# Performance work log

Hardware: AMD Instinct MI355X
Metric: run time of the kernel (lower is better)

## Reference

```python
import jax, jax.numpy as jnp
import numpy as np
import math

E = 65536        # neighbor pairs (edges)
NAT = 2048       # atoms
NRAD = 24        # radial basis size
ZETA = [1, 2, 3, 4]
NCOMP = len(ZETA) + 1  # radial components: one 2-body + one per zeta
RCUT = 6.0
NELEM = 94       # one-hot element encoding size
EMB = 16         # species embedding dim


def _tables():
    """Static lxlylz enumeration per zeta: triples with lx+ly+lz = n, n in 0..z,
    multinomial/binomial normalization and (-1)^n lambda sign."""
    f = np.vectorize(math.factorial)
    tabs = []
    for z in ZETA:
        L = []
        for n in range(z + 1):
            for lx in range(n + 1):
                for ly in range(n - lx + 1):
                    L.append((lx, ly, n - lx - ly))
        L = np.array(L, np.int64)              # [K,3]
        nsum = L.sum(1)                        # [K]
        fact_lxlylz = f(L[:, 0]) * f(L[:, 1]) * f(L[:, 2])
        # (nfact/fact_lxlylz) * z!/((z-n)! n!) = z! / ((z-n)! * lx!ly!lz!)
        fact_norm = math.factorial(z) / (f(z - nsum) * fact_lxlylz)
        lam = (-1.0) ** nsum
        tabs.append((jnp.asarray(L, jnp.float32),
                     jnp.asarray(fact_norm, jnp.float32),
                     jnp.asarray(lam, jnp.float32)))
    return tabs

TABS = _tables()


def _forward(rij, Wr1, br1, Wr2, br2, Ws1, bs1, Ws2, bs2,
             Wa1, ba1, Wa2, ba2, Wa3, ba3, first_atom_idx, species_idx):
    nat = species_idx.shape[0]
    r = jnp.linalg.norm(rij, axis=1)                       # [E]
    u = rij / r[:, None]                                   # [E,3] unit vectors
    fc = 0.5 * (jnp.cos(jnp.pi * jnp.minimum(r, RCUT) / RCUT) + 1.0)
    centers = jnp.linspace(0.0, RCUT, NRAD, dtype=jnp.float32)
    width = RCUT / NRAD
    basis = jnp.exp(-((r[:, None] - centers) ** 2) / (2.0 * width * width)) * fc[:, None]  # [E,NRAD]
    # learned radial functions -> [E, NRAD, NCOMP]
    h = jax.nn.silu(basis @ Wr1 + br1)
    radial = jax.nn.silu(h @ Wr2 + br2).reshape(-1, NRAD, NCOMP)
    seg = first_atom_idx
    # two-body descriptor
    feats = [jax.ops.segment_sum(radial[:, :, 0], seg, num_segments=nat)]  # [nat,NRAD]
    for iz, z in enumerate(ZETA):
        L, fnorm, lam = TABS[iz]
        # g_ij over lxlylz combos: prod of powers of unit-vector components
        g_ij = jnp.prod((u[:, None, :] + 1e-12) ** L[None, :, :], axis=-1) * fnorm  # [E,K]
        g = jnp.einsum('er,ek->erk', radial[:, :, iz + 1], g_ij)                    # [E,NRAD,K]
        gi = jax.ops.segment_sum(g, seg, num_segments=nat)                          # [nat,NRAD,K]
        g2 = gi * gi
        norm = 2.0 ** (1.0 - z)
        feats.append(jnp.sum(g2, axis=-1) * norm)          # lambda = +1
        feats.append(jnp.sum(g2 * lam, axis=-1) * norm)    # lambda = -1
    feat = jnp.concatenate(feats, axis=1)                  # [nat, NRAD*(1+2*nzeta)]
    # species embedding and correlation
    onehot = jax.nn.one_hot(species_idx, NELEM, dtype=feat.dtype)
    emb = jax.nn.silu(onehot @ Ws1 + bs1) @ Ws2 + bs2      # [nat,EMB]
    x = (feat[:, :, None] * emb[:, None, :]).reshape(nat, -1)  # [nat, F*EMB]
    h = jax.nn.silu(x @ Wa1 + ba1)
    h = jax.nn.silu(h @ Wa2 + ba2)
    e = h @ Wa3 + ba3                                      # [nat,1] atomic energies
    return jnp.sum(e)                                      # total energy


def setup_inputs() -> dict:
    key = jax.random.key(0)
    ks = jax.random.split(key, 12)
    def w(k, shp):
        return jax.random.normal(k, shp, jnp.float32) / np.float32(np.sqrt(shp[0]))
    F = NRAD * (1 + 2 * len(ZETA)) * EMB  # 3456
    return {
        "rij": jax.random.normal(ks[0], (E, 3), jnp.float32) * 2.0,
        "Wr1": w(ks[1], (NRAD, 64)), "br1": jnp.zeros((64,), jnp.float32),
        "Wr2": w(ks[2], (64, NCOMP * NRAD)), "br2": jnp.zeros((NCOMP * NRAD,), jnp.float32),
        "Ws1": w(ks[3], (NELEM, 32)), "bs1": jnp.zeros((32,), jnp.float32),
        "Ws2": w(ks[4], (32, EMB)), "bs2": jnp.zeros((EMB,), jnp.float32),
        "Wa1": w(ks[5], (F, 256)), "ba1": jnp.zeros((256,), jnp.float32),
        "Wa2": w(ks[6], (256, 128)), "ba2": jnp.zeros((128,), jnp.float32),
        "Wa3": w(ks[7], (128, 1)), "ba3": jnp.zeros((1,), jnp.float32),
        "first_atom_idx": jnp.sort(jax.random.randint(ks[8], (E,), 0, NAT)),
        "species_idx": jax.random.randint(ks[9], (NAT,), 0, NELEM),
    }


def reference(rij, Wr1, br1, Wr2, br2, Ws1, bs1, Ws2, bs2,
              Wa1, ba1, Wa2, ba2, Wa3, ba3, first_atom_idx, species_idx):
    return _forward(rij, Wr1, br1, Wr2, br2, Ws1, bs1, Ws2, bs2,
                    Wa1, ba1, Wa2, ba2, Wa3, ba3, first_atom_idx, species_idx)
```

## Files before the change

### kernel.cpp

```cpp
#include <hip/hip_runtime.h>
#include <math.h>

#define KTOT 69
#define NRADC 24
#define NFEAT 216
#define NELEMC 94
#define EMBC 16
#define H1C 256
#define H2C 128
#define CE 16
#define EPR 20
#define KGN 18
#define GSTR 84
#define GISTR 76
#define TA 8
#define NPT 344

__device__ __constant__ int c_lx[KTOT] = {
  0,0,0,1,
  0,0,0,1,0,0,0,1,1,2,
  0,0,0,1,0,0,0,1,1,2,0,0,0,0,1,1,1,2,2,3,
  0,0,0,1,0,0,0,1,1,2,0,0,0,0,1,1,1,2,2,3,0,0,0,0,0,1,1,1,1,2,2,2,3,3,4};
__device__ __constant__ int c_ly[KTOT] = {
  0,0,1,0,
  0,0,1,0,0,1,2,0,1,0,
  0,0,1,0,0,1,2,0,1,0,0,1,2,3,0,1,2,0,1,0,
  0,0,1,0,0,1,2,0,1,0,0,1,2,3,0,1,2,0,1,0,0,1,2,3,4,0,1,2,3,0,1,2,0,1,0};
__device__ __constant__ int c_lz[KTOT] = {
  0,1,0,0,
  0,1,0,0,2,1,0,1,0,0,
  0,1,0,0,2,1,0,1,0,0,3,2,1,0,2,1,0,1,0,0,
  0,1,0,0,2,1,0,1,0,0,3,2,1,0,2,1,0,1,0,0,4,3,2,1,0,3,2,1,0,2,1,0,1,0,0};
__device__ __constant__ float c_fn[KTOT] = {
  1,1,1,1,
  1,2,2,2,1,2,1,2,2,1,
  1,3,3,3,3,6,3,6,6,3,1,3,3,1,3,6,3,3,3,1,
  1,4,4,4,6,12,6,12,12,6,4,12,12,4,12,24,12,12,12,4,
  1,4,6,4,1,4,12,12,4,6,12,6,4,4,1};
__device__ __constant__ float c_lam[KTOT] = {
  1,-1,-1,-1,
  1,-1,-1,-1,1,1,1,1,1,1,
  1,-1,-1,-1,1,1,1,1,1,1,-1,-1,-1,-1,-1,-1,-1,-1,-1,-1,
  1,-1,-1,-1,1,1,1,1,1,1,-1,-1,-1,-1,-1,-1,-1,-1,-1,-1,
  1,1,1,1,1,1,1,1,1,1,1,1,1,1,1};
__device__ __constant__ int c_k0[4] = {0,4,14,34};
__device__ __constant__ int c_kn[4] = {4,10,20,35};
__device__ __constant__ float c_zn[4] = {1.0f, 0.5f, 0.25f, 0.125f};
__device__ __constant__ int c_zidg[KGN] = {0, 1,1,1, 2,2,2,2,2, 3,3,3,3,3,3,3,3,3};

__device__ __forceinline__ float silu(float x) { return x / (1.0f + expf(-x)); }
__device__ __forceinline__ float4 silu4(float4 v) {
  v.x = silu(v.x); v.y = silu(v.y); v.z = silu(v.z); v.w = silu(v.w); return v;
}
__device__ __forceinline__ void fma4(float4& a, float s, const float4 w) {
  a.x += s * w.x; a.y += s * w.y; a.z += s * w.z; a.w += s * w.w;
}
__device__ __forceinline__ void fma44(float4& a, const float4 x, const float4 y) {
  a.x += x.x * y.x; a.y += x.y * y.y; a.z += x.z * y.z; a.w += x.w * y.w;
}
__device__ __forceinline__ float hsum4(const float4 v) { return (v.x + v.y) + (v.z + v.w); }
__device__ __forceinline__ float powsel(int l, float p, float p2, float p3, float p4) {
  float v = 1.0f;
  v = l >= 1 ? p : v;
  v = l >= 2 ? p2 : v;
  v = l >= 3 ? p3 : v;
  v = l >= 4 ? p4 : v;
  return v;
}

__global__ __launch_bounds__(256) void k_prep(
    const int* __restrict__ fai, const int* __restrict__ spc,
    const float* __restrict__ Ws1, const float* __restrict__ bs1,
    const float* __restrict__ Ws2, const float* __restrict__ bs2,
    const float* __restrict__ Wa1,
    int* __restrict__ bounds, int* __restrict__ porder,
    float* __restrict__ B, int E, int nat, int nbB) {
  const int blk = blockIdx.x;
  const int tid = threadIdx.x;
  __shared__ float s_hh[24 * 32];
  __shared__ float s_emb[24 * EMBC];
  __shared__ int s_cnt[NELEMC];
  __shared__ int s_off[NELEMC];

  if (blk < nbB) {
    int e = blk * 256 + tid;
    if (e < E) {
      int f = fai[e];
      int fp = (e == 0) ? -1 : fai[e - 1];
      for (int a = fp + 1; a <= f; ++a) bounds[a] = e;
      if (e == E - 1)
        for (int a = f + 1; a <= nat; ++a) bounds[a] = E;
    }
  } else if (blk == nbB) {
    for (int i = tid; i < NELEMC; i += 256) s_cnt[i] = 0;
    __syncthreads();
    for (int a = tid; a < nat; a += 256) atomicAdd(&s_cnt[spc[a]], 1);
    __syncthreads();
    if (tid == 0) {
      int run = 0;
      for (int s = 0; s < NELEMC; ++s) {
        s_off[s] = run;
        run += ((s_cnt[s] + TA - 1) / TA) * TA;
      }
    }
    for (int i = tid; i < NPT * TA; i += 256) porder[i] = -1;
    __syncthreads();
    for (int a = tid; a < nat; a += 256) {
      int pos = atomicAdd(&s_off[spc[a]], 1);
      porder[pos] = a;
    }
  } else {
    const int bi = blk - nbB - 1;
    const int i = bi >> 2;
    const int sc0 = (bi & 3) * 24;
    const int scn = min(NELEMC, sc0 + 24) - sc0;
    const int o = tid;
    for (int idx = tid; idx < scn * 32; idx += 256) {
      int s = idx >> 5, c = idx & 31;
      s_hh[idx] = silu(Ws1[(sc0 + s) * 32 + c] + bs1[c]);
    }
    __syncthreads();
    for (int idx = tid; idx < scn * EMBC; idx += 256) {
      int s = idx >> 4, j = idx & 15;
      float acc = bs2[j];
      #pragma unroll
      for (int c = 0; c < 32; ++c) acc += s_hh[s * 32 + c] * Ws2[c * EMBC + j];
      s_emb[idx] = acc;
    }
    __syncthreads();
    float w[EMBC];
    #pragma unroll
    for (int j = 0; j < EMBC; ++j) w[j] = Wa1[(size_t)(i * EMBC + j) * H1C + o];
    for (int s = 0; s < scn; ++s) {
      float acc = 0.0f;
      #pragma unroll
      for (int j = 0; j < EMBC; ++j) acc += s_emb[s * EMBC + j] * w[j];
      B[((size_t)(sc0 + s) * NFEAT + i) * H1C + o] = acc;
    }
  }
}

template <int NQ>
__device__ __forceinline__ void edge_l2(
    const float* __restrict__ s_h, const float* __restrict__ Wr2,
    const float* __restrict__ br2, float4* __restrict__ radial4,
    int e, int og, int eg, int E) {
  float4 acc[NQ];
  const float4* b2 = (const float4*)(br2 + og * 32);
  #pragma unroll
  for (int q = 0; q < NQ; ++q) acc[q] = b2[q];
  #pragma unroll 8
  for (int j = 0; j < 64; ++j) {
    float hv = s_h[e * 65 + j];
    const float4* w = (const float4*)(Wr2 + j * 120 + og * 32);
    #pragma unroll
    for (int q = 0; q < NQ; ++q) fma4(acc[q], hv, w[q]);
  }
  if (eg < E) {
    #pragma unroll
    for (int q = 0; q < NQ; ++q)
      radial4[(size_t)eg * 30 + og * 8 + q] = silu4(acc[q]);
  }
}

__global__ __launch_bounds__(256) void k_edge(
    const float* __restrict__ rij,
    const float* __restrict__ Wr1, const float* __restrict__ br1,
    const float* __restrict__ Wr2, const float* __restrict__ br2,
    float4* __restrict__ radial4, int E) {
  __shared__ float s_bas[64 * 25];
  __shared__ float s_h[64 * 65];
  const int tid = threadIdx.x;
  const int e = tid & 63;
  const int og = __builtin_amdgcn_readfirstlane(tid >> 6);
  const int eg = blockIdx.x * 64 + e;

  {
    float x = 0.0f, y = 0.0f, z = 0.0f;
    const bool ev = eg < E;
    if (ev) { x = rij[3 * eg]; y = rij[3 * eg + 1]; z = rij[3 * eg + 2]; }
    float r = sqrtf(x * x + y * y + z * z);
    float fcv = ev ? 0.5f * (cosf(3.14159265358979323846f * fminf(r, 6.0f) *
                                  (1.0f / 6.0f)) + 1.0f)
                   : 0.0f;
    #pragma unroll
    for (int t = 0; t < 6; ++t) {
      int m = og * 6 + t;
      float d = r - (6.0f / 23.0f) * (float)m;
      s_bas[e * 25 + m] = expf(-8.0f * d * d) * fcv;
    }
  }
  __syncthreads();

  {
    const float4* b1 = (const float4*)(br1 + og * 16);
    float4 acc[4] = {b1[0], b1[1], b1[2], b1[3]};
    #pragma unroll 8
    for (int m = 0; m < NRADC; ++m) {
      float b = s_bas[e * 25 + m];
      const float4* w = (const float4*)(Wr1 + m * 64 + og * 16);
      #pragma unroll
      for (int q = 0; q < 4; ++q) fma4(acc[q], b, w[q]);
    }
    #pragma unroll
    for (int q = 0; q < 4; ++q) {
      float4 v = silu4(acc[q]);
      float* dst = &s_h[e * 65 + og * 16 + 4 * q];
      dst[0] = v.x; dst[1] = v.y; dst[2] = v.z; dst[3] = v.w;
    }
  }
  __syncthreads();

  if (og < 3) edge_l2<8>(s_h, Wr2, br2, radial4, e, og, eg, E);
  else        edge_l2<6>(s_h, Wr2, br2, radial4, e, og, eg, E);
}

__global__ __launch_bounds__(256) void k_atom(
    const float* __restrict__ rij,
    const float4* __restrict__ radial4,
    const int* __restrict__ bounds,
    float* __restrict__ feat, int E) {
  const int a = blockIdx.x;
  const int tid = threadIdx.x;
  __shared__ __align__(16) float s_radT[120 * EPR];
  __shared__ __align__(16) float s_gijT[KGN * GSTR];
  __shared__ __align__(16) float s_gi[NRADC * GISTR];
  __shared__ float s_feat[NFEAT];

  const int start = bounds[a];
  const int end = bounds[a + 1];

  const int e = tid & 15;
  const int sub = tid >> 4;

  const bool is_tile = tid < 216;
  const int eh = (tid < 216) ? (tid / 108) : 0;
  const int tile = (tid < 216) ? (tid % 108) : 0;
  const int rg = tile % 6;
  const int kg = tile / 6;
  const int comp0 = rg * 20 + 1 + c_zidg[kg];
  const bool is_2b = (tid >= 216 && tid < 240);
  const int rad2b = tid - 216;

  const int kstart = sub < 5 ? sub * 5 : 25 + (sub - 5) * 4;
  const int kcnt = sub < 5 ? 5 : 4;
  int t_pk[5], t_addr[5]; float t_fn[5];
  #pragma unroll
  for (int t = 0; t < 5; ++t) {
    int k = (t < kcnt) ? kstart + t : 0;
    t_pk[t] = c_lx[k] | (c_ly[k] << 8) | (c_lz[k] << 16);
    t_fn[t] = c_fn[k];
    int prow = k + (k < 14 ? 0 : 2);
    t_addr[t] = (prow >> 2) * GSTR + (prow & 3) * EPR + e;
  }

  const int pe0 = tid / 30, pc0 = tid - pe0 * 30;
  const int pe1 = (tid + 256) / 30, pc1 = (tid + 256) - pe1 * 30;

  if (tid < 60) {
    int rr = tid / EPR, ec = tid % EPR;
    int fkg = rr < 2 ? 3 : 17;
    int fj = rr < 2 ? 2 + rr : 3;
    s_gijT[fkg * GSTR + fj * EPR + ec] = 0.0f;
  }

  float4 acc[4][4];
  #pragma unroll
  for (int i = 0; i < 4; ++i)
    #pragma unroll
    for (int j = 0; j < 4; ++j) acc[i][j] = make_float4(0, 0, 0, 0);
  float4 acc2b = make_float4(0, 0, 0, 0);

  float4 pfA, pfB;
  float rx, ry, rz;
  auto prefetch = [&](int c0) {
    int lim = (end - c0) * 30;
    pfA = make_float4(0, 0, 0, 0);
    pfB = make_float4(0, 0, 0, 0);
    if (tid < lim) pfA = radial4[(size_t)c0 * 30 + tid];
    if (tid < 224 && tid + 256 < lim) pfB = radial4[(size_t)c0 * 30 + 256 + tid];
    int eg = c0 + e;
    rx = 0.0f; ry = 0.0f; rz = 0.0f;
    if (eg < end) { rx = rij[3 * eg]; ry = rij[3 * eg + 1]; rz = rij[3 * eg + 2]; }
  };
  prefetch(start);

  for (int c0 = start; c0 < end; c0 += CE) {
    __syncthreads();
    {
      int c = pc0 * 4;
      s_radT[(c + 0) * EPR + pe0] = pfA.x;
      s_radT[(c + 1) * EPR + pe0] = pfA.y;
      s_radT[(c + 2) * EPR + pe0] = pfA.z;
      s_radT[(c + 3) * EPR + pe0] = pfA.w;
      if (tid < 224) {
        int c2 = pc1 * 4;
        s_radT[(c2 + 0) * EPR + pe1] = pfB.x;
        s_radT[(c2 + 1) * EPR + pe1] = pfB.y;
        s_radT[(c2 + 2) * EPR + pe1] = pfB.z;
        s_radT[(c2 + 3) * EPR + pe1] = pfB.w;
      }
    }
    {
      const bool ev = (c0 + e) < end;
      float r = sqrtf(rx * rx + ry * ry + rz * rz);
      float inv = 1.0f / r;
      float px = rx * inv + 1e-12f, py = ry * inv + 1e-12f, pz = rz * inv + 1e-12f;
      float p2x = px * px, p3x = p2x * px, p4x = p2x * p2x;
      float p2y = py * py, p3y = p2y * py, p4y = p2y * p2y;
      float p2z = pz * pz, p3z = p2z * pz, p4z = p2z * p2z;
      #pragma unroll
      for (int t = 0; t < 5; ++t) {
        if (t < kcnt) {
          int pk = t_pk[t];
          float g = powsel(pk & 0xff, px, p2x, p3x, p4x) *
                    powsel((pk >> 8) & 0xff, py, p2y, p3y, p4y) *
                    powsel(pk >> 16, pz, p2z, p3z, p4z) * t_fn[t];
          s_gijT[t_addr[t]] = ev ? g : 0.0f;
        }
      }
    }
    __syncthreads();
    prefetch(c0 + CE);
    if (is_tile) {
      #pragma unroll
      for (int s = 0; s < 2; ++s) {
        int e0 = eh * 8 + s * 4;
        float4 gg[4];
        #pragma unroll
        for (int j = 0; j < 4; ++j)
          gg[j] = *(const float4*)&s_gijT[kg * GSTR + j * EPR + e0];
        #pragma unroll
        for (int i = 0; i < 4; ++i) {
          float4 rr = *(const float4*)&s_radT[(comp0 + 5 * i) * EPR + e0];
          #pragma unroll
          for (int j = 0; j < 4; ++j) fma44(acc[i][j], rr, gg[j]);
        }
      }
    }
    if (is_2b) {
      #pragma unroll
      for (int e0 = 0; e0 < 16; e0 += 4) {
        float4 v = *(const float4*)&s_radT[(rad2b * 5) * EPR + e0];
        acc2b.x += v.x; acc2b.y += v.y; acc2b.z += v.z; acc2b.w += v.w;
      }
    }
  }

  float4 hs[4];
  #pragma unroll
  for (int i = 0; i < 4; ++i)
    hs[i] = make_float4(hsum4(acc[i][0]), hsum4(acc[i][1]),
                        hsum4(acc[i][2]), hsum4(acc[i][3]));
  __syncthreads();
  if (is_tile && eh == 0) {
    #pragma unroll
    for (int i = 0; i < 4; ++i)
      *(float4*)&s_gi[(rg * 4 + i) * GISTR + kg * 4] = hs[i];
  }
  if (is_2b) s_feat[rad2b] = hsum4(acc2b);
  __syncthreads();
  if (is_tile && eh == 1) {
    #pragma unroll
    for (int i = 0; i < 4; ++i) {
      float4 v = *(const float4*)&s_gi[(rg * 4 + i) * GISTR + kg * 4];
      v.x += hs[i].x; v.y += hs[i].y; v.z += hs[i].z; v.w += hs[i].w;
      *(float4*)&s_gi[(rg * 4 + i) * GISTR + kg * 4] = v;
    }
  }
  __syncthreads();

  if (tid < 192) {
    int zb = tid / NRADC;
    int rad = tid - zb * NRADC;
    int z = zb >> 1;
    bool neg = zb & 1;
    int k0 = c_k0[z], kn = c_kn[z];
    float s = 0.0f;
    for (int k = k0; k < k0 + kn; ++k) {
      int prow = k + (k < 14 ? 0 : 2);
      float g = s_gi[rad * GISTR + prow];
      float g2 = g * g;
      s += neg ? g2 * c_lam[k] : g2;
    }
    s_feat[NRADC + zb * NRADC + rad] = s * c_zn[z];
  }
  __syncthreads();
  if (tid < NFEAT) feat[(size_t)a * NFEAT + tid] = s_feat[tid];
}

__global__ __launch_bounds__(256) void k_mlp1(
    const float* __restrict__ feat, const float* __restrict__ B,
    const float* __restrict__ ba1, const int* __restrict__ porder,
    const int* __restrict__ sp, float* __restrict__ h1) {
  const int nb = gridDim.x;
  int blk = blockIdx.x;
  if ((nb & 7) == 0) blk = (blockIdx.x & 7) * (nb >> 3) + (blockIdx.x >> 3);
  const int r0 = blk * TA;
  const int o = threadIdx.x;
  __shared__ int s_a[TA];
  __shared__ __align__(16) float s_fT[NFEAT * TA];
  if (o < TA) s_a[o] = porder[r0 + o];
  __syncthreads();
  if (s_a[0] < 0) return;
  const int s = sp[s_a[0]];
  for (int idx = o; idx < TA * 54; idx += 256) {
    int u = idx / 54, q = idx - u * 54;
    int a = s_a[u];
    float4 v = make_float4(0, 0, 0, 0);
    if (a >= 0) v = *(const float4*)(feat + (size_t)a * NFEAT + q * 4);
    s_fT[(q * 4 + 0) * TA + u] = v.x;
    s_fT[(q * 4 + 1) * TA + u] = v.y;
    s_fT[(q * 4 + 2) * TA + u] = v.z;
    s_fT[(q * 4 + 3) * TA + u] = v.w;
  }
  __syncthreads();
  float4 A0 = make_float4(0, 0, 0, 0), A1 = make_float4(0, 0, 0, 0);
  const float* Bp = B + ((size_t)s * NFEAT) * H1C + o;
  #pragma unroll 4
  for (int i = 0; i < NFEAT; ++i) {
    float bv = Bp[(size_t)i * H1C];
    float4 f0 = *(const float4*)&s_fT[i * TA];
    float4 f1 = *(const float4*)&s_fT[i * TA + 4];
    fma4(A0, bv, f0);
    fma4(A1, bv, f1);
  }
  const float b1v = ba1[o];
  float hv[TA] = {A0.x, A0.y, A0.z, A0.w, A1.x, A1.y, A1.z, A1.w};
  #pragma unroll
  for (int u = 0; u < TA; ++u)
    h1[(size_t)(r0 + u) * H1C + o] = silu(hv[u] + b1v);
}

__global__ __launch_bounds__(256) void k_mlp2(
    const float* __restrict__ h1, const float* __restrict__ Wa2,
    const float* __restrict__ ba2, const float* __restrict__ Wa3,
    const float* __restrict__ ba3, const int* __restrict__ porder,
    float* __restrict__ e_out) {
  const int nb = gridDim.x;
  int blk = blockIdx.x;
  if ((nb & 7) == 0) blk = (blockIdx.x & 7) * (nb >> 3) + (blockIdx.x >> 3);
  const int r0 = blk * TA;
  const int tid = threadIdx.x;
  const int o = tid & 127;
  const int half = tid >> 7;
  __shared__ int s_a[TA];
  __shared__ __align__(16) float s_hT[H1C * TA];
  __shared__ float s_pre[TA][132];
  __shared__ float s_val[TA][132];
  if (tid < TA) s_a[tid] = porder[r0 + tid];
  __syncthreads();
  if (s_a[0] < 0) return;
  for (int idx = tid; idx < TA * 64; idx += 256) {
    int u = idx >> 6, q = idx & 63;
    float4 v = *(const float4*)(h1 + (size_t)(r0 + u) * H1C + q * 4);
    s_hT[(q * 4 + 0) * TA + u] = v.x;
    s_hT[(q * 4 + 1) * TA + u] = v.y;
    s_hT[(q * 4 + 2) * TA + u] = v.z;
    s_hT[(q * 4 + 3) * TA + u] = v.w;
  }
  __syncthreads();
  float4 A0 = make_float4(0, 0, 0, 0), A1 = make_float4(0, 0, 0, 0);
  const int j0 = half * 128;
  #pragma unroll 4
  for (int j = j0; j < j0 + 128; ++j) {
    float wv = Wa2[j * H2C + o];
    float4 h0 = *(const float4*)&s_hT[j * TA];
    float4 hb = *(const float4*)&s_hT[j * TA + 4];
    fma4(A0, wv, h0);
    fma4(A1, wv, hb);
  }
  float pa[TA] = {A0.x, A0.y, A0.z, A0.w, A1.x, A1.y, A1.z, A1.w};
  if (half == 0) {
    #pragma unroll
    for (int u = 0; u < TA; ++u) s_pre[u][o] = pa[u];
  }
  __syncthreads();
  if (half == 1) {
    float b = ba2[o], w3 = Wa3[o];
    #pragma unroll
    for (int u = 0; u < TA; ++u)
      s_val[u][o] = silu(s_pre[u][o] + pa[u] + b) * w3;
  }
  __syncthreads();
  if (tid < TA) {
    int a = s_a[tid];
    if (a >= 0) {
      float ss = 0.0f;
      for (int k = 0; k < H2C; ++k) ss += s_val[tid][k];
      e_out[a] = ss + ba3[0];
    }
  }
}

__global__ void k_reduce(const float* __restrict__ e_in, float* __restrict__ out, int nat) {
  int t = threadIdx.x;
  double acc = 0.0;
  for (int i = t; i < nat; i += 256) acc += (double)e_in[i];
  for (int o = 32; o; o >>= 1) acc += __shfl_down(acc, o, 64);
  __shared__ double s_par[4];
  if ((t & 63) == 0) s_par[t >> 6] = acc;
  __syncthreads();
  if (t == 0) out[0] = (float)(s_par[0] + s_par[1] + s_par[2] + s_par[3]);
}

extern "C" void kernel_launch(void* const* d_in, const int* in_sizes, int n_in,
                              void* d_out, int out_size, void* d_ws, size_t ws_size,
                              hipStream_t stream) {
  const float* rij = (const float*)d_in[0];
  const float* Wr1 = (const float*)d_in[1];
  const float* br1 = (const float*)d_in[2];
  const float* Wr2 = (const float*)d_in[3];
  const float* br2 = (const float*)d_in[4];
  const float* Ws1 = (const float*)d_in[5];
  const float* bs1 = (const float*)d_in[6];
  const float* Ws2 = (const float*)d_in[7];
  const float* bs2 = (const float*)d_in[8];
  const float* Wa1 = (const float*)d_in[9];
  const float* ba1 = (const float*)d_in[10];
  const float* Wa2 = (const float*)d_in[11];
  const float* ba2 = (const float*)d_in[12];
  const float* Wa3 = (const float*)d_in[13];
  const float* ba3 = (const float*)d_in[14];
  const int* fai = (const int*)d_in[15];
  const int* spc = (const int*)d_in[16];

  const int E = in_sizes[0] / 3;
  const int nat = in_sizes[16];

  float* ws = (float*)d_ws;
  size_t off = 0;
  float* radial = ws + off; off += (size_t)E * 120;
  float* feat = ws + off;  off += (size_t)nat * NFEAT;
  float* Bm = ws + off;    off += (size_t)NELEMC * NFEAT * H1C;
  float* h1 = ws + off;    off += (size_t)NPT * TA * H1C;
  float* e_ws = ws + off;  off += (size_t)nat;
  int* porder = (int*)(ws + off); off += (size_t)NPT * TA;
  int* bounds = (int*)(ws + off);

  const int nbB = (E + 255) / 256;
  k_prep<<<nbB + 1 + NFEAT * 4, 256, 0, stream>>>(fai, spc, Ws1, bs1, Ws2, bs2,
                                                  Wa1, bounds, porder, Bm, E, nat,
                                                  nbB);
  k_edge<<<(E + 63) / 64, 256, 0, stream>>>(rij, Wr1, br1, Wr2, br2,
                                            (float4*)radial, E);
  k_atom<<<nat, 256, 0, stream>>>(rij, (const float4*)radial, bounds, feat, E);
  k_mlp1<<<NPT, 256, 0, stream>>>(feat, Bm, ba1, porder, spc, h1);
  k_mlp2<<<NPT, 256, 0, stream>>>(h1, Wa2, ba2, Wa3, ba3, porder, e_ws);
  k_reduce<<<1, 256, 0, stream>>>(e_ws, (float*)d_out, nat);
}
```

Baseline: 208.3 us.

## Merge prep and edge kernels into one launch and fuse two MLP layers

The prep work (segment bounds, species ordering, embedding-folded first-layer weights) now runs as extra blocks of the edge radial-MLP kernel, so the independent preprocessing overlaps with edge work and one launch goes away. The first and second atom MLP layers are fused into one kernel that keeps the hidden layer in shared memory instead of writing and rereading it from global memory. This cuts launch gaps and global traffic for h1. In exchange the fused MLP kernel uses more shared memory per block, which may lower occupancy.

```diff
diff --git a/kernel.cpp b/kernel.cpp
--- a/kernel.cpp
+++ b/kernel.cpp
@@ -68,78 +68,6 @@
   return v;
 }
 
-__global__ __launch_bounds__(256) void k_prep(
-    const int* __restrict__ fai, const int* __restrict__ spc,
-    const float* __restrict__ Ws1, const float* __restrict__ bs1,
-    const float* __restrict__ Ws2, const float* __restrict__ bs2,
-    const float* __restrict__ Wa1,
-    int* __restrict__ bounds, int* __restrict__ porder,
-    float* __restrict__ B, int E, int nat, int nbB) {
-  const int blk = blockIdx.x;
-  const int tid = threadIdx.x;
-  __shared__ float s_hh[24 * 32];
-  __shared__ float s_emb[24 * EMBC];
-  __shared__ int s_cnt[NELEMC];
-  __shared__ int s_off[NELEMC];
-
-  if (blk < nbB) {
-    int e = blk * 256 + tid;
-    if (e < E) {
-      int f = fai[e];
-      int fp = (e == 0) ? -1 : fai[e - 1];
-      for (int a = fp + 1; a <= f; ++a) bounds[a] = e;
-      if (e == E - 1)
-        for (int a = f + 1; a <= nat; ++a) bounds[a] = E;
-    }
-  } else if (blk == nbB) {
-    for (int i = tid; i < NELEMC; i += 256) s_cnt[i] = 0;
-    __syncthreads();
-    for (int a = tid; a < nat; a += 256) atomicAdd(&s_cnt[spc[a]], 1);
-    __syncthreads();
-    if (tid == 0) {
-      int run = 0;
-      for (int s = 0; s < NELEMC; ++s) {
-        s_off[s] = run;
-        run += ((s_cnt[s] + TA - 1) / TA) * TA;
-      }
-    }
-    for (int i = tid; i < NPT * TA; i += 256) porder[i] = -1;
-    __syncthreads();
-    for (int a = tid; a < nat; a += 256) {
-      int pos = atomicAdd(&s_off[spc[a]], 1);
-      porder[pos] = a;
-    }
-  } else {
-    const int bi = blk - nbB - 1;
-    const int i = bi >> 2;
-    const int sc0 = (bi & 3) * 24;
-    const int scn = min(NELEMC, sc0 + 24) - sc0;
-    const int o = tid;
-    for (int idx = tid; idx < scn * 32; idx += 256) {
-      int s = idx >> 5, c = idx & 31;
-      s_hh[idx] = silu(Ws1[(sc0 + s) * 32 + c] + bs1[c]);
-    }
-    __syncthreads();
-    for (int idx = tid; idx < scn * EMBC; idx += 256) {
-      int s = idx >> 4, j = idx & 15;
-      float acc = bs2[j];
-      #pragma unroll
-      for (int c = 0; c < 32; ++c) acc += s_hh[s * 32 + c] * Ws2[c * EMBC + j];
-      s_emb[idx] = acc;
-    }
-    __syncthreads();
-    float w[EMBC];
-    #pragma unroll
-    for (int j = 0; j < EMBC; ++j) w[j] = Wa1[(size_t)(i * EMBC + j) * H1C + o];
-    for (int s = 0; s < scn; ++s) {
-      float acc = 0.0f;
-      #pragma unroll
-      for (int j = 0; j < EMBC; ++j) acc += s_emb[s * EMBC + j] * w[j];
-      B[((size_t)(sc0 + s) * NFEAT + i) * H1C + o] = acc;
-    }
-  }
-}
-
 template <int NQ>
 __device__ __forceinline__ void edge_l2(
     const float* __restrict__ s_h, const float* __restrict__ Wr2,
@@ -163,56 +91,123 @@
   }
 }
 
-__global__ __launch_bounds__(256) void k_edge(
+__global__ __launch_bounds__(256) void k_front(
     const float* __restrict__ rij,
     const float* __restrict__ Wr1, const float* __restrict__ br1,
     const float* __restrict__ Wr2, const float* __restrict__ br2,
-    float4* __restrict__ radial4, int E) {
-  __shared__ float s_bas[64 * 25];
-  __shared__ float s_h[64 * 65];
+    const int* __restrict__ fai, const int* __restrict__ spc,
+    const float* __restrict__ Ws1, const float* __restrict__ bs1,
+    const float* __restrict__ Ws2, const float* __restrict__ bs2,
+    const float* __restrict__ Wa1,
+    float4* __restrict__ radial4, int* __restrict__ bounds,
+    int* __restrict__ porder, float* __restrict__ B,
+    int E, int nat, int nbE, int nbB) {
+  __shared__ __align__(16) float s_mem[64 * 25 + 64 * 65];
+  const int blk = blockIdx.x;
   const int tid = threadIdx.x;
-  const int e = tid & 63;
-  const int og = __builtin_amdgcn_readfirstlane(tid >> 6);
-  const int eg = blockIdx.x * 64 + e;
-
-  {
-    float x = 0.0f, y = 0.0f, z = 0.0f;
-    const bool ev = eg < E;
-    if (ev) { x = rij[3 * eg]; y = rij[3 * eg + 1]; z = rij[3 * eg + 2]; }
-    float r = sqrtf(x * x + y * y + z * z);
-    float fcv = ev ? 0.5f * (cosf(3.14159265358979323846f * fminf(r, 6.0f) *
-                                  (1.0f / 6.0f)) + 1.0f)
-                   : 0.0f;
+
+  if (blk < nbE) {
+    float* s_bas = s_mem;
+    float* s_h = s_mem + 64 * 25;
+    const int e = tid & 63;
+    const int og = __builtin_amdgcn_readfirstlane(tid >> 6);
+    const int eg = blk * 64 + e;
+    {
+      float x = 0.0f, y = 0.0f, z = 0.0f;
+      const bool ev = eg < E;
+      if (ev) { x = rij[3 * eg]; y = rij[3 * eg + 1]; z = rij[3 * eg + 2]; }
+      float r = sqrtf(x * x + y * y + z * z);
+      float fcv = ev ? 0.5f * (cosf(3.14159265358979323846f * fminf(r, 6.0f) *
+                                    (1.0f / 6.0f)) + 1.0f)
+                     : 0.0f;
+      #pragma unroll
+      for (int t = 0; t < 6; ++t) {
+        int m = og * 6 + t;
+        float d = r - (6.0f / 23.0f) * (float)m;
+        s_bas[e * 25 + m] = expf(-8.0f * d * d) * fcv;
+      }
+    }
+    __syncthreads();
+    {
+      const float4* b1 = (const float4*)(br1 + og * 16);
+      float4 acc[4] = {b1[0], b1[1], b1[2], b1[3]};
+      #pragma unroll 8
+      for (int m = 0; m < NRADC; ++m) {
+        float b = s_bas[e * 25 + m];
+        const float4* w = (const float4*)(Wr1 + m * 64 + og * 16);
+        #pragma unroll
+        for (int q = 0; q < 4; ++q) fma4(acc[q], b, w[q]);
+      }
+      #pragma unroll
+      for (int q = 0; q < 4; ++q) {
+        float4 v = silu4(acc[q]);
+        float* dst = &s_h[e * 65 + og * 16 + 4 * q];
+        dst[0] = v.x; dst[1] = v.y; dst[2] = v.z; dst[3] = v.w;
+      }
+    }
+    __syncthreads();
+    if (og < 3) edge_l2<8>(s_h, Wr2, br2, radial4, e, og, eg, E);
+    else        edge_l2<6>(s_h, Wr2, br2, radial4, e, og, eg, E);
+  } else if (blk < nbE + nbB) {
+    int e = (blk - nbE) * 256 + tid;
+    if (e < E) {
+      int f = fai[e];
+      int fp = (e == 0) ? -1 : fai[e - 1];
+      for (int a = fp + 1; a <= f; ++a) bounds[a] = e;
+      if (e == E - 1)
+        for (int a = f + 1; a <= nat; ++a) bounds[a] = E;
+    }
+  } else if (blk == nbE + nbB) {
+    int* s_cnt = (int*)s_mem;
+    int* s_off = s_cnt + NELEMC;
+    for (int i = tid; i < NELEMC; i += 256) s_cnt[i] = 0;
+    __syncthreads();
+    for (int a = tid; a < nat; a += 256) atomicAdd(&s_cnt[spc[a]], 1);
+    __syncthreads();
+    if (tid == 0) {
+      int run = 0;
+      for (int s = 0; s < NELEMC; ++s) {
+        s_off[s] = run;
+        run += ((s_cnt[s] + TA - 1) / TA) * TA;
+      }
+    }
+    for (int i = tid; i < NPT * TA; i += 256) porder[i] = -1;
+    __syncthreads();
+    for (int a = tid; a < nat; a += 256) {
+      int pos = atomicAdd(&s_off[spc[a]], 1);
+      porder[pos] = a;
+    }
+  } else {
+    float* s_hh = s_mem;
+    float* s_emb = s_mem + 24 * 32;
+    const int bi = blk - (nbE + nbB + 1);
+    const int i = bi >> 2;
+    const int sc0 = (bi & 3) * 24;
+    const int scn = min(NELEMC, sc0 + 24) - sc0;
+    const int o = tid;
+    for (int idx = tid; idx < scn * 32; idx += 256) {
+      int s = idx >> 5, c = idx & 31;
+      s_hh[idx] = silu(Ws1[(sc0 + s) * 32 + c] + bs1[c]);
+    }
+    __syncthreads();
+    for (int idx = tid; idx < scn * EMBC; idx += 256) {
+      int s = idx >> 4, j = idx & 15;
+      float acc = bs2[j];
+      #pragma unroll
+      for (int c = 0; c < 32; ++c) acc += s_hh[s * 32 + c] * Ws2[c * EMBC + j];
+      s_emb[idx] = acc;
+    }
+    __syncthreads();
+    float w[EMBC];
     #pragma unroll
-    for (int t = 0; t < 6; ++t) {
-      int m = og * 6 + t;
-      float d = r - (6.0f / 23.0f) * (float)m;
-      s_bas[e * 25 + m] = expf(-8.0f * d * d) * fcv;
-    }
-  }
-  __syncthreads();
-
-  {
-    const float4* b1 = (const float4*)(br1 + og * 16);
-    float4 acc[4] = {b1[0], b1[1], b1[2], b1[3]};
-    #pragma unroll 8
-    for (int m = 0; m < NRADC; ++m) {
-      float b = s_bas[e * 25 + m];
-      const float4* w = (const float4*)(Wr1 + m * 64 + og * 16);
-      #pragma unroll
-      for (int q = 0; q < 4; ++q) fma4(acc[q], b, w[q]);
-    }
-    #pragma unroll
-    for (int q = 0; q < 4; ++q) {
-      float4 v = silu4(acc[q]);
-      float* dst = &s_h[e * 65 + og * 16 + 4 * q];
-      dst[0] = v.x; dst[1] = v.y; dst[2] = v.z; dst[3] = v.w;
-    }
-  }
-  __syncthreads();
-
-  if (og < 3) edge_l2<8>(s_h, Wr2, br2, radial4, e, og, eg, E);
-  else        edge_l2<6>(s_h, Wr2, br2, radial4, e, og, eg, E);
+    for (int j = 0; j < EMBC; ++j) w[j] = Wa1[(size_t)(i * EMBC + j) * H1C + o];
+    for (int s = 0; s < scn; ++s) {
+      float acc = 0.0f;
+      #pragma unroll
+      for (int j = 0; j < EMBC; ++j) acc += s_emb[s * EMBC + j] * w[j];
+      B[((size_t)(sc0 + s) * NFEAT + i) * H1C + o] = acc;
+    }
+  }
 }
 
 __global__ __launch_bounds__(256) void k_atom(
@@ -389,22 +384,27 @@
   if (tid < NFEAT) feat[(size_t)a * NFEAT + tid] = s_feat[tid];
 }
 
-__global__ __launch_bounds__(256) void k_mlp1(
+__global__ __launch_bounds__(256) void k_mlp(
     const float* __restrict__ feat, const float* __restrict__ B,
-    const float* __restrict__ ba1, const int* __restrict__ porder,
-    const int* __restrict__ sp, float* __restrict__ h1) {
+    const float* __restrict__ ba1, const float* __restrict__ Wa2,
+    const float* __restrict__ ba2, const float* __restrict__ Wa3,
+    const float* __restrict__ ba3, const int* __restrict__ porder,
+    const int* __restrict__ sp, float* __restrict__ e_out) {
   const int nb = gridDim.x;
   int blk = blockIdx.x;
   if ((nb & 7) == 0) blk = (blockIdx.x & 7) * (nb >> 3) + (blockIdx.x >> 3);
   const int r0 = blk * TA;
-  const int o = threadIdx.x;
+  const int tid = threadIdx.x;
   __shared__ int s_a[TA];
   __shared__ __align__(16) float s_fT[NFEAT * TA];
-  if (o < TA) s_a[o] = porder[r0 + o];
+  __shared__ __align__(16) float s_hT[H1C * TA];
+  __shared__ float s_pre[TA][132];
+  __shared__ float s_val[TA][132];
+  if (tid < TA) s_a[tid] = porder[r0 + tid];
   __syncthreads();
   if (s_a[0] < 0) return;
   const int s = sp[s_a[0]];
-  for (int idx = o; idx < TA * 54; idx += 256) {
+  for (int idx = tid; idx < TA * 54; idx += 256) {
     int u = idx / 54, q = idx - u * 54;
     int a = s_a[u];
     float4 v = make_float4(0, 0, 0, 0);
@@ -415,72 +415,50 @@
     s_fT[(q * 4 + 3) * TA + u] = v.w;
   }
   __syncthreads();
-  float4 A0 = make_float4(0, 0, 0, 0), A1 = make_float4(0, 0, 0, 0);
-  const float* Bp = B + ((size_t)s * NFEAT) * H1C + o;
-  #pragma unroll 4
-  for (int i = 0; i < NFEAT; ++i) {
-    float bv = Bp[(size_t)i * H1C];
-    float4 f0 = *(const float4*)&s_fT[i * TA];
-    float4 f1 = *(const float4*)&s_fT[i * TA + 4];
-    fma4(A0, bv, f0);
-    fma4(A1, bv, f1);
-  }
-  const float b1v = ba1[o];
-  float hv[TA] = {A0.x, A0.y, A0.z, A0.w, A1.x, A1.y, A1.z, A1.w};
-  #pragma unroll
-  for (int u = 0; u < TA; ++u)
-    h1[(size_t)(r0 + u) * H1C + o] = silu(hv[u] + b1v);
-}
-
-__global__ __launch_bounds__(256) void k_mlp2(
-    const float* __restrict__ h1, const float* __restrict__ Wa2,
-    const float* __restrict__ ba2, const float* __restrict__ Wa3,
-    const float* __restrict__ ba3, const int* __restrict__ porder,
-    float* __restrict__ e_out) {
-  const int nb = gridDim.x;
-  int blk = blockIdx.x;
-  if ((nb & 7) == 0) blk = (blockIdx.x & 7) * (nb >> 3) + (blockIdx.x >> 3);
-  const int r0 = blk * TA;
-  const int tid = threadIdx.x;
-  const int o = tid & 127;
-  const int half = tid >> 7;
-  __shared__ int s_a[TA];
-  __shared__ __align__(16) float s_hT[H1C * TA];
-  __shared__ float s_pre[TA][132];
-  __shared__ float s_val[TA][132];
-  if (tid < TA) s_a[tid] = porder[r0 + tid];
-  __syncthreads();
-  if (s_a[0] < 0) return;
-  for (int idx = tid; idx < TA * 64; idx += 256) {
-    int u = idx >> 6, q = idx & 63;
-    float4 v = *(const float4*)(h1 + (size_t)(r0 + u) * H1C + q * 4);
-    s_hT[(q * 4 + 0) * TA + u] = v.x;
-    s_hT[(q * 4 + 1) * TA + u] = v.y;
-    s_hT[(q * 4 + 2) * TA + u] = v.z;
-    s_hT[(q * 4 + 3) * TA + u] = v.w;
-  }
-  __syncthreads();
-  float4 A0 = make_float4(0, 0, 0, 0), A1 = make_float4(0, 0, 0, 0);
-  const int j0 = half * 128;
-  #pragma unroll 4
-  for (int j = j0; j < j0 + 128; ++j) {
-    float wv = Wa2[j * H2C + o];
-    float4 h0 = *(const float4*)&s_hT[j * TA];
-    float4 hb = *(const float4*)&s_hT[j * TA + 4];
-    fma4(A0, wv, h0);
-    fma4(A1, wv, hb);
-  }
-  float pa[TA] = {A0.x, A0.y, A0.z, A0.w, A1.x, A1.y, A1.z, A1.w};
-  if (half == 0) {
-    #pragma unroll
-    for (int u = 0; u < TA; ++u) s_pre[u][o] = pa[u];
-  }
-  __syncthreads();
-  if (half == 1) {
-    float b = ba2[o], w3 = Wa3[o];
-    #pragma unroll
-    for (int u = 0; u < TA; ++u)
-      s_val[u][o] = silu(s_pre[u][o] + pa[u] + b) * w3;
+  {
+    const int o = tid;
+    float4 A0 = make_float4(0, 0, 0, 0), A1 = make_float4(0, 0, 0, 0);
+    const float* Bp = B + ((size_t)s * NFEAT) * H1C + o;
+    #pragma unroll 4
+    for (int i = 0; i < NFEAT; ++i) {
+      float bv = Bp[(size_t)i * H1C];
+      float4 f0 = *(const float4*)&s_fT[i * TA];
+      float4 f1 = *(const float4*)&s_fT[i * TA + 4];
+      fma4(A0, bv, f0);
+      fma4(A1, bv, f1);
+    }
+    const float b1v = ba1[o];
+    *(float4*)&s_hT[o * TA] = silu4(make_float4(A0.x + b1v, A0.y + b1v,
+                                                A0.z + b1v, A0.w + b1v));
+    *(float4*)&s_hT[o * TA + 4] = silu4(make_float4(A1.x + b1v, A1.y + b1v,
+                                                    A1.z + b1v, A1.w + b1v));
+  }
+  __syncthreads();
+  {
+    const int o = tid & 127;
+    const int half = tid >> 7;
+    float4 A0 = make_float4(0, 0, 0, 0), A1 = make_float4(0, 0, 0, 0);
+    const int j0 = half * 128;
+    #pragma unroll 4
+    for (int j = j0; j < j0 + 128; ++j) {
+      float wv = Wa2[j * H2C + o];
+      float4 h0 = *(const float4*)&s_hT[j * TA];
+      float4 hb = *(const float4*)&s_hT[j * TA + 4];
+      fma4(A0, wv, h0);
+      fma4(A1, wv, hb);
+    }
+    float pa[TA] = {A0.x, A0.y, A0.z, A0.w, A1.x, A1.y, A1.z, A1.w};
+    if (half == 0) {
+      #pragma unroll
+      for (int u = 0; u < TA; ++u) s_pre[u][o] = pa[u];
+    }
+    __syncthreads();
+    if (half == 1) {
+      float b = ba2[o], w3 = Wa3[o];
+      #pragma unroll
+      for (int u = 0; u < TA; ++u)
+        s_val[u][o] = silu(s_pre[u][o] + pa[u] + b) * w3;
+    }
   }
   __syncthreads();
   if (tid < TA) {
@@ -533,19 +511,17 @@
   float* radial = ws + off; off += (size_t)E * 120;
   float* feat = ws + off;  off += (size_t)nat * NFEAT;
   float* Bm = ws + off;    off += (size_t)NELEMC * NFEAT * H1C;
-  float* h1 = ws + off;    off += (size_t)NPT * TA * H1C;
   float* e_ws = ws + off;  off += (size_t)nat;
   int* porder = (int*)(ws + off); off += (size_t)NPT * TA;
   int* bounds = (int*)(ws + off);
 
+  const int nbE = (E + 63) / 64;
   const int nbB = (E + 255) / 256;
-  k_prep<<<nbB + 1 + NFEAT * 4, 256, 0, stream>>>(fai, spc, Ws1, bs1, Ws2, bs2,
-                                                  Wa1, bounds, porder, Bm, E, nat,
-                                                  nbB);
-  k_edge<<<(E + 63) / 64, 256, 0, stream>>>(rij, Wr1, br1, Wr2, br2,
-                                            (float4*)radial, E);
+  k_front<<<nbE + nbB + 1 + NFEAT * 4, 256, 0, stream>>>(
+      rij, Wr1, br1, Wr2, br2, fai, spc, Ws1, bs1, Ws2, bs2, Wa1,
+      (float4*)radial, bounds, porder, Bm, E, nat, nbE, nbB);
   k_atom<<<nat, 256, 0, stream>>>(rij, (const float4*)radial, bounds, feat, E);
-  k_mlp1<<<NPT, 256, 0, stream>>>(feat, Bm, ba1, porder, spc, h1);
-  k_mlp2<<<NPT, 256, 0, stream>>>(h1, Wa2, ba2, Wa3, ba3, porder, e_ws);
+  k_mlp<<<NPT, 256, 0, stream>>>(feat, Bm, ba1, Wa2, ba2, Wa3, ba3,
+                                 porder, spc, e_ws);
   k_reduce<<<1, 256, 0, stream>>>(e_ws, (float*)d_out, nat);
 }
```

Result: faster. 197.6 us (-5.2%).
